# Optimization experiments

Hardware: AMD Instinct MI355X
Metric: run time of the kernel (lower is better)

The kernel has to match this reference:

```python
import jax, jax.numpy as jnp
import numpy as np
import math

DIM = 384; HEADS = 12; HD = 32; L_REL = 4; L_STD = 12; MLP_H = 4 * DIM
B = 8; N = 256
N_REL = 1
TIME_SCALE = 30000.0 / 500 * 0.3
SCALE = HD ** -0.5
NEG = -1e9  # finite stand-in for -inf padding mask (identical softmax result, safe grads)


def _ln(x, g, b):
    m = x.mean(-1, keepdims=True)
    v = ((x - m) ** 2).mean(-1, keepdims=True)
    return (x - m) / jnp.sqrt(v + 1e-5) * g + b


def _sin_emb(x, dim):
    half = dim // 2
    freq = jnp.exp(jnp.arange(half, dtype=x.dtype) * (-math.log(10000.0) / half))
    e = x[..., None] * freq
    return jnp.concatenate([jnp.sin(e), jnp.cos(e)], -1)


def _rel_bias(x0, w1d, b1d, wp, bp):
    pos = x0[..., :3]
    t = x0[..., 3:4]
    dpos = pos[:, :, None] - pos[:, None, :]                 # [B,N,N,3]
    dt = t[:, :, None] - t[:, None, :] * TIME_SCALE          # [B,N,N,1] (scale on 2nd term, as in torch)
    dpos2 = dpos ** 2
    dt2 = dt ** 2
    ds2 = dpos2.sum(-1) - dt2[..., 0]
    d = jnp.sign(ds2) * jnp.sqrt(jnp.abs(ds2))
    f = jnp.concatenate([dpos, dt, dpos2, dt2], -1)          # [B,N,N,8]
    d = d + (f @ w1d.T + b1d)[..., 0]
    emb = _sin_emb(1024.0 * jnp.clip(d, -4.0, 4.0), HD)      # [B,N,N,HD]
    return emb @ wp.T + bp


def _mask_bias(mask):
    mn = jnp.minimum(mask[:, None, :], mask[:, :, None])
    mx = jnp.maximum(mask[:, None, :], mask[:, :, None])
    return jnp.where(mx < 0, 0.0, mn)                        # [B,N,N]


def _attn(xq, xkv, wq, wk, wv, wo, bo, rel, mbias):
    Bq, Nq, _ = xq.shape
    q = (xq @ wq.T).reshape(Bq, Nq, HEADS, HD).transpose(0, 2, 1, 3) * SCALE
    k = (xkv @ wk.T).reshape(Bq, Nq, HEADS, HD).transpose(0, 2, 1, 3)
    v = (xkv @ wv.T).reshape(Bq, Nq, HEADS, HD).transpose(0, 2, 1, 3)
    a = jnp.einsum('bhic,bhjc->bhij', q, k)
    if rel is not None:
        a = a + jnp.einsum('bhic,bijc->bhij', q, rel)
    if mbias is not None:
        a = a + mbias[:, None]
    a = jax.nn.softmax(a, axis=-1)
    o = jnp.einsum('bhij,bhjc->bihc', a, v)
    if rel is not None:
        o = o + jnp.einsum('bhij,bijc->bihc', a, rel)
    return o.reshape(Bq, Nq, HEADS * HD) @ wo.T + bo


def _mlp(x, w1, b1, w2, b2):
    return jax.nn.gelu(x @ w1.T + b1, approximate=False) @ w2.T + b2


def setup_inputs() -> dict:
    key = jax.random.key(0)
    ks = iter(jax.random.split(key, 64))
    f = lambda shape: jax.random.normal(next(ks), shape, jnp.float32) * 0.02
    inp = {}
    inp['x'] = jax.random.normal(next(ks), (B, N, DIM), jnp.float32)
    inp['x0'] = jax.random.normal(next(ks), (B, N, 4), jnp.float32)
    lengths = jax.random.randint(next(ks), (B,), N // 2, N + 1)
    inp['mask'] = jnp.where(jnp.arange(N)[None, :] < lengths[:, None], 0.0, NEG).astype(jnp.float32)
    inp['rp_w1d'] = f((1, 8)); inp['rp_b1d'] = jnp.zeros((1,), jnp.float32)
    inp['rp_wp'] = f((HD, HD)); inp['rp_bp'] = jnp.zeros((HD,), jnp.float32)
    for p, L in (('sw', L_REL), ('bl', L_STD)):
        inp[p + '_ln1_g'] = jnp.ones((L, DIM), jnp.float32); inp[p + '_ln1_b'] = jnp.zeros((L, DIM), jnp.float32)
        inp[p + '_ln2_g'] = jnp.ones((L, DIM), jnp.float32); inp[p + '_ln2_b'] = jnp.zeros((L, DIM), jnp.float32)
        inp[p + '_wq'] = f((L, DIM, DIM)); inp[p + '_wk'] = f((L, DIM, DIM)); inp[p + '_wv'] = f((L, DIM, DIM))
        inp[p + '_wo'] = f((L, DIM, DIM)); inp[p + '_bo'] = jnp.zeros((L, DIM), jnp.float32)
        inp[p + '_w1'] = f((L, MLP_H, DIM)); inp[p + '_b1'] = jnp.zeros((L, MLP_H), jnp.float32)
        inp[p + '_w2'] = f((L, DIM, MLP_H)); inp[p + '_b2'] = jnp.zeros((L, DIM), jnp.float32)
    inp['bl_g1'] = jnp.ones((L_STD, DIM), jnp.float32)   # init_values=1
    inp['bl_g2'] = jnp.ones((L_STD, DIM), jnp.float32)
    inp['cls_w'] = f((DIM,))
    inp['out_w'] = f((3, DIM)); inp['out_b'] = jnp.zeros((3,), jnp.float32)
    return inp


def reference(x, x0, mask, rp_w1d, rp_b1d, rp_wp, rp_bp,
              sw_ln1_g, sw_ln1_b, sw_ln2_g, sw_ln2_b, sw_wq, sw_wk, sw_wv, sw_wo, sw_bo,
              sw_w1, sw_b1, sw_w2, sw_b2,
              bl_ln1_g, bl_ln1_b, bl_ln2_g, bl_ln2_b, bl_wq, bl_wk, bl_wv, bl_wo, bl_bo,
              bl_w1, bl_b1, bl_w2, bl_b2, bl_g1, bl_g2, cls_w, out_w, out_b):
    rel = _rel_bias(x0, rp_w1d, rp_b1d, rp_wp, rp_bp)
    mbias = _mask_bias(mask)
    for i in range(L_REL):
        r = rel if i < N_REL else None
        xn = _ln(x, sw_ln1_g[i], sw_ln1_b[i])
        x = x + _attn(xn, xn, sw_wq[i], sw_wk[i], sw_wv[i], sw_wo[i], sw_bo[i], r, mbias)
        x = x + _mlp(_ln(x, sw_ln2_g[i], sw_ln2_b[i]), sw_w1[i], sw_b1[i], sw_w2[i], sw_b2[i])
    # prepend cls token; it is always valid
    cls = jnp.broadcast_to(cls_w[None, None, :], (x.shape[0], 1, DIM))
    x = jnp.concatenate([cls, x], axis=1)
    mask2 = jnp.concatenate([jnp.zeros((x.shape[0], 1), mask.dtype), mask], axis=1)
    mbias2 = _mask_bias(mask2)
    for i in range(L_STD):
        xn = _ln(x, bl_ln1_g[i], bl_ln1_b[i])
        x = x + bl_g1[i] * _attn(xn, xn, bl_wq[i], bl_wk[i], bl_wv[i], bl_wo[i], bl_bo[i], None, mbias2)
        x = x + bl_g2[i] * _mlp(_ln(x, bl_ln2_g[i], bl_ln2_b[i]), bl_w1[i], bl_b1[i], bl_w2[i], bl_b2[i])
    return x[:, 0] @ out_w.T + out_b   # [B, 3]
```

## Files before the change

kernel.cpp:

```cpp
#include <hip/hip_runtime.h>
#include <hip/hip_bf16.h>
#include <math.h>

#define DIM 384
#define HEADS 12
#define HD 32
#define MLP_H 1536
#define BATCH 8
#define N1 256
#define N2 257
#define QP 1152
#define SCALE 0.17677669529663687f
#define TIME_SCALE 18.0f

typedef __attribute__((ext_vector_type(8))) short frag8;
typedef __attribute__((ext_vector_type(4))) float f32x4;

__device__ inline short f2bf(float x) {
    __hip_bfloat16 h = __float2bfloat16(x);
    short s;
    __builtin_memcpy(&s, &h, 2);
    return s;
}
__device__ inline float bf2f(short s) {
    unsigned u = ((unsigned)(unsigned short)s) << 16;
    float f;
    __builtin_memcpy(&f, &u, 4);
    return f;
}

__global__ __launch_bounds__(256) void conv_kernel(
        const float* __restrict__ in, short* __restrict__ out, int n) {
    int i = (blockIdx.x * 256 + threadIdx.x) * 4;
    if (i >= n) return;
    float4 v = *(const float4*)(in + i);
    out[i]     = f2bf(v.x);
    out[i + 1] = f2bf(v.y);
    out[i + 2] = f2bf(v.z);
    out[i + 3] = f2bf(v.w);
}

__global__ __launch_bounds__(256) void conv_qkv_kernel(
        const float* __restrict__ wq, const float* __restrict__ wk,
        const float* __restrict__ wv, short* __restrict__ out, int L) {
    size_t idx = ((size_t)blockIdx.x * 256 + threadIdx.x) * 4;
    size_t total = (size_t)L * QP * DIM;
    if (idx >= total) return;
    size_t k = idx % DIM;
    size_t row = idx / DIM;
    size_t r = row % QP;
    size_t l = row / QP;
    int which = (int)(r / DIM);
    int rr = (int)(r % DIM);
    const float* src = ((which == 0) ? wq : (which == 1) ? wk : wv)
                     + (l * DIM + rr) * DIM + k;
    float4 v = *(const float4*)src;
    out[idx]     = f2bf(v.x);
    out[idx + 1] = f2bf(v.y);
    out[idx + 2] = f2bf(v.z);
    out[idx + 3] = f2bf(v.w);
}

__global__ __launch_bounds__(256) void rel_kernel(
        const float* __restrict__ x0, const float* __restrict__ w1d,
        const float* __restrict__ b1d, const float* __restrict__ wp,
        const float* __restrict__ bp, short* __restrict__ rel) {
    __shared__ float swp[HD * HD];
    __shared__ float sbp[HD];
    __shared__ float sw1[8];
    __shared__ float sb1;
    __shared__ float sfreq[16];
    int tid = threadIdx.x;
    for (int i = tid; i < HD * HD; i += 256) swp[i] = wp[i];
    if (tid < HD) sbp[tid] = bp[tid];
    if (tid < 8) sw1[tid] = w1d[tid];
    if (tid == 0) sb1 = b1d[0];
    if (tid < 16) sfreq[tid] = expf(-(float)tid * 0.5756462732485114f);
    __syncthreads();

    int gid = blockIdx.x * 256 + tid;
    int j  = gid & (N1 - 1);
    int bi = gid >> 8;
    int i  = bi & (N1 - 1);
    int b  = bi >> 8;

    const float* pi = x0 + (size_t)(b * N1 + i) * 4;
    const float* pj = x0 + (size_t)(b * N1 + j) * 4;
    float dx = pi[0] - pj[0], dy = pi[1] - pj[1], dz = pi[2] - pj[2];
    float dt = pi[3] - pj[3] * TIME_SCALE;
    float dx2 = dx * dx, dy2 = dy * dy, dz2 = dz * dz, dt2 = dt * dt;
    float ds2 = dx2 + dy2 + dz2 - dt2;
    float d = copysignf(sqrtf(fabsf(ds2)), ds2);
    d += dx * sw1[0] + dy * sw1[1] + dz * sw1[2] + dt * sw1[3]
       + dx2 * sw1[4] + dy2 * sw1[5] + dz2 * sw1[6] + dt2 * sw1[7] + sb1;
    d = fminf(fmaxf(d, -4.f), 4.f) * 1024.f;

    float emb[32];
    #pragma unroll
    for (int k = 0; k < 16; k++) {
        float s, c;
        sincosf(d * sfreq[k], &s, &c);
        emb[k] = s; emb[16 + k] = c;
    }
    short* out = rel + (size_t)gid * HD;
    #pragma unroll 4
    for (int c = 0; c < HD; c++) {
        float a = sbp[c];
        #pragma unroll
        for (int k = 0; k < 32; k++) a += emb[k] * swp[c * 32 + k];
        out[c] = f2bf(a);
    }
}

__global__ __launch_bounds__(128) void ln_kernel(
        const float* __restrict__ x, const float* __restrict__ g,
        const float* __restrict__ b, short* __restrict__ y) {
    int r = blockIdx.x;
    int t = threadIdx.x;
    const float* xr = x + (size_t)r * DIM;
    float v0 = xr[t], v1 = xr[t + 128], v2 = xr[t + 256];
    __shared__ float redm[2], redv[2];
    float s = v0 + v1 + v2;
    for (int o = 32; o; o >>= 1) s += __shfl_down(s, o, 64);
    int lane = t & 63, wid = t >> 6;
    if (!lane) redm[wid] = s;
    __syncthreads();
    float mean = (redm[0] + redm[1]) * (1.f / DIM);
    float d0 = v0 - mean, d1 = v1 - mean, d2 = v2 - mean;
    float s2 = d0 * d0 + d1 * d1 + d2 * d2;
    for (int o = 32; o; o >>= 1) s2 += __shfl_down(s2, o, 64);
    if (!lane) redv[wid] = s2;
    __syncthreads();
    float var = (redv[0] + redv[1]) * (1.f / DIM);
    float rs = rsqrtf(var + 1e-5f);
    short* yr = y + (size_t)r * DIM;
    yr[t]       = f2bf(d0 * rs * g[t]       + b[t]);
    yr[t + 128] = f2bf(d1 * rs * g[t + 128] + b[t + 128]);
    yr[t + 256] = f2bf(d2 * rs * g[t + 256] + b[t + 256]);
}

__global__ __launch_bounds__(512) void gemm_bf16_kernel(
        const short* __restrict__ A, const short* __restrict__ W,
        const float* __restrict__ bias, const float* __restrict__ resid,
        const float* __restrict__ gvec, float* __restrict__ Cf,
        short* __restrict__ Cb, int M, int Np, int K, int mode) {
    __shared__ short As2[2][2][4][64][8];
    __shared__ short Bs2[2][2][4][64][8];
    int tid = threadIdx.x;
    int w = tid >> 6, lane = tid & 63;
    int nlo = lane & 15, quad = lane >> 4;
    int g = w >> 2, wl = w & 3;
    int wm = wl >> 1, wn = wl & 1;
    int n0 = blockIdx.x * 64, m0 = blockIdx.y * 64;

    f32x4 acc00 = {0.f, 0.f, 0.f, 0.f}, acc01 = {0.f, 0.f, 0.f, 0.f};
    f32x4 acc10 = {0.f, 0.f, 0.f, 0.f}, acc11 = {0.f, 0.f, 0.f, 0.f};

    int oct16 = tid & 15, rbase = tid >> 4;
    int kh_s = oct16 >> 3, oo = oct16 & 7, ks_s = oo >> 2, q_s = oo & 3;
    const frag8 fz = {0, 0, 0, 0, 0, 0, 0, 0};
    frag8 pa0 = fz, pa1 = fz, pb0, pb1;

    {
        int gm0 = m0 + rbase, gm1 = m0 + rbase + 32;
        if (gm0 < M) pa0 = *(const frag8*)(A + (size_t)gm0 * K + oct16 * 8);
        if (gm1 < M) pa1 = *(const frag8*)(A + (size_t)gm1 * K + oct16 * 8);
        pb0 = *(const frag8*)(W + (size_t)(n0 + rbase) * K + oct16 * 8);
        pb1 = *(const frag8*)(W + (size_t)(n0 + rbase + 32) * K + oct16 * 8);
    }

    for (int k0 = 0; k0 < K; k0 += 128) {
        *(frag8*)&As2[kh_s][ks_s][q_s][rbase][0]      = pa0;
        *(frag8*)&As2[kh_s][ks_s][q_s][rbase + 32][0] = pa1;
        *(frag8*)&Bs2[kh_s][ks_s][q_s][rbase][0]      = pb0;
        *(frag8*)&Bs2[kh_s][ks_s][q_s][rbase + 32][0] = pb1;
        __syncthreads();
        int kn = k0 + 128;
        if (kn < K) {
            int gm0 = m0 + rbase, gm1 = m0 + rbase + 32;
            pa0 = fz; pa1 = fz;
            if (gm0 < M) pa0 = *(const frag8*)(A + (size_t)gm0 * K + kn + oct16 * 8);
            if (gm1 < M) pa1 = *(const frag8*)(A + (size_t)gm1 * K + kn + oct16 * 8);
            pb0 = *(const frag8*)(W + (size_t)(n0 + rbase) * K + kn + oct16 * 8);
            pb1 = *(const frag8*)(W + (size_t)(n0 + rbase + 32) * K + kn + oct16 * 8);
        }
        #pragma unroll
        for (int ks = 0; ks < 2; ks++) {
            frag8 a0 = *(const frag8*)&As2[g][ks][quad][wm * 32 + nlo][0];
            frag8 a1 = *(const frag8*)&As2[g][ks][quad][wm * 32 + 16 + nlo][0];
            frag8 b0 = *(const frag8*)&Bs2[g][ks][quad][wn * 32 + nlo][0];
            frag8 b1 = *(const frag8*)&Bs2[g][ks][quad][wn * 32 + 16 + nlo][0];
            acc00 = __builtin_amdgcn_mfma_f32_16x16x32_bf16(a0, b0, acc00, 0, 0, 0);
            acc01 = __builtin_amdgcn_mfma_f32_16x16x32_bf16(a0, b1, acc01, 0, 0, 0);
            acc10 = __builtin_amdgcn_mfma_f32_16x16x32_bf16(a1, b0, acc10, 0, 0, 0);
            acc11 = __builtin_amdgcn_mfma_f32_16x16x32_bf16(a1, b1, acc11, 0, 0, 0);
        }
        __syncthreads();
    }

    f32x4* red4 = (f32x4*)&As2[0][0][0][0][0];
    int roff = wl * 64 + lane;
    if (g == 1) {
        red4[roff]       = acc00;
        red4[256 + roff] = acc01;
        red4[512 + roff] = acc10;
        red4[768 + roff] = acc11;
    }
    __syncthreads();
    if (g == 1) return;
    {
        f32x4 t0 = red4[roff], t1 = red4[256 + roff];
        f32x4 t2 = red4[512 + roff], t3 = red4[768 + roff];
        #pragma unroll
        for (int r = 0; r < 4; r++) {
            acc00[r] += t0[r]; acc01[r] += t1[r];
            acc10[r] += t2[r]; acc11[r] += t3[r];
        }
    }

    #pragma unroll
    for (int mi = 0; mi < 2; mi++) {
        #pragma unroll
        for (int nf = 0; nf < 2; nf++) {
            f32x4 av = (mi == 0) ? ((nf == 0) ? acc00 : acc01)
                                 : ((nf == 0) ? acc10 : acc11);
            int col = n0 + wn * 32 + nf * 16 + nlo;
            float bcol = (mode >= 1) ? bias[col] : 0.f;
            float gs = 1.f;
            if (mode == 2 && gvec) gs = gvec[col];
            #pragma unroll
            for (int r = 0; r < 4; r++) {
                int row = m0 + wm * 32 + mi * 16 + quad * 4 + r;
                if (row >= M) continue;
                float v = av[r] + bcol;
                if (mode == 1) v = 0.5f * v * (1.f + erff(v * 0.70710678118654752f));
                if (mode == 2) {
                    Cf[(size_t)row * Np + col] = resid[(size_t)row * Np + col] + gs * v;
                } else {
                    Cb[(size_t)row * Np + col] = f2bf(v);
                }
            }
        }
    }
}

__global__ __launch_bounds__(256) void attn_mfma_kernel(
        const short* __restrict__ qkv, const float* __restrict__ maskv,
        short* __restrict__ ob, int Nseq) {
    __shared__ short kf[18][64][8];
    __shared__ short vf[9][2][64][8];
    __shared__ short pbuf[4][16][40];
    __shared__ float ms[320];

    int tid = threadIdx.x;
    int w = tid >> 6, lane = tid & 63;
    int n = lane & 15, quad = lane >> 4;
    int qg = blockIdx.x, h = blockIdx.y, b = blockIdx.z;
    size_t rowB = (size_t)(b * Nseq);

    for (int j = tid; j < 320; j += 256)
        ms[j] = (j < Nseq) ? maskv[b * Nseq + j] : 0.f;

    {
        int c0 = (tid & 3) * 8;
        for (int j = tid >> 2; j < 288; j += 64) {
            frag8 kk = {0, 0, 0, 0, 0, 0, 0, 0};
            frag8 vv = {0, 0, 0, 0, 0, 0, 0, 0};
            if (j < Nseq) {
                const short* base = qkv + (rowB + j) * QP + h * HD + c0;
                kk = *(const frag8*)(base + 384);
                vv = *(const frag8*)(base + 768);
            }
            *(frag8*)&kf[j >> 4][(c0 >> 3) * 16 + (j & 15)][0] = kk;
            #pragma unroll
            for (int e = 0; e < 8; e++) {
                int c = c0 + e;
                vf[j >> 5][c >> 4][((j & 31) >> 3) * 16 + (c & 15)][j & 7] = vv[e];
            }
        }
    }

    int i0 = qg * 64 + w * 16;
    frag8 qa = {0, 0, 0, 0, 0, 0, 0, 0};
    {
        int i = i0 + n;
        if (i < Nseq) qa = *(const frag8*)(qkv + (rowB + i) * QP + h * HD + quad * 8);
    }
    __syncthreads();

    float msq[4];
    #pragma unroll
    for (int r = 0; r < 4; r++) msq[r] = ms[i0 + quad * 4 + r];

    float mrow[4], lsum[4];
    #pragma unroll
    for (int r = 0; r < 4; r++) { mrow[r] = -3.0e38f; lsum[r] = 0.f; }
    f32x4 oacc0 = {0.f, 0.f, 0.f, 0.f}, oacc1 = {0.f, 0.f, 0.f, 0.f};

    for (int jb = 0; jb < 9; jb++) {
        frag8 kb0 = *(const frag8*)&kf[2 * jb][lane][0];
        frag8 kb1 = *(const frag8*)&kf[2 * jb + 1][lane][0];
        f32x4 z = {0.f, 0.f, 0.f, 0.f};
        f32x4 s0 = __builtin_amdgcn_mfma_f32_16x16x32_bf16(qa, kb0, z, 0, 0, 0);
        f32x4 s1 = __builtin_amdgcn_mfma_f32_16x16x32_bf16(qa, kb1, z, 0, 0, 0);

        int j0 = jb * 32 + n;
        int j1 = j0 + 16;
        float mj0 = ms[j0], mj1 = ms[j1];
        float pad0 = (j0 < Nseq) ? 0.f : -1e9f;
        float pad1 = (j1 < Nseq) ? 0.f : -1e9f;

        #pragma unroll
        for (int r = 0; r < 4; r++) {
            float mi = msq[r];
            float b0 = ((fmaxf(mi, mj0) < 0.f) ? 0.f : fminf(mi, mj0)) + pad0;
            float b1 = ((fmaxf(mi, mj1) < 0.f) ? 0.f : fminf(mi, mj1)) + pad1;
            float v0 = s0[r] * SCALE + b0;
            float v1 = s1[r] * SCALE + b1;
            float rm = fmaxf(v0, v1);
            rm = fmaxf(rm, __shfl_xor(rm, 1));
            rm = fmaxf(rm, __shfl_xor(rm, 2));
            rm = fmaxf(rm, __shfl_xor(rm, 4));
            rm = fmaxf(rm, __shfl_xor(rm, 8));
            float mn = fmaxf(mrow[r], rm);
            float alpha = __expf(mrow[r] - mn);
            mrow[r] = mn;
            float p0 = __expf(v0 - mn);
            float p1 = __expf(v1 - mn);
            float ps = p0 + p1;
            ps += __shfl_xor(ps, 1);
            ps += __shfl_xor(ps, 2);
            ps += __shfl_xor(ps, 4);
            ps += __shfl_xor(ps, 8);
            lsum[r] = lsum[r] * alpha + ps;
            oacc0[r] *= alpha;
            oacc1[r] *= alpha;
            pbuf[w][quad * 4 + r][n]      = f2bf(p0);
            pbuf[w][quad * 4 + r][n + 16] = f2bf(p1);
        }
        __syncthreads();
        frag8 pa = *(const frag8*)&pbuf[w][n][quad * 8];
        frag8 vb0 = *(const frag8*)&vf[jb][0][lane][0];
        frag8 vb1 = *(const frag8*)&vf[jb][1][lane][0];
        oacc0 = __builtin_amdgcn_mfma_f32_16x16x32_bf16(pa, vb0, oacc0, 0, 0, 0);
        oacc1 = __builtin_amdgcn_mfma_f32_16x16x32_bf16(pa, vb1, oacc1, 0, 0, 0);
        __syncthreads();
    }

    #pragma unroll
    for (int r = 0; r < 4; r++) {
        int i = i0 + quad * 4 + r;
        if (i < Nseq) {
            float invl = 1.f / lsum[r];
            ob[(rowB + i) * DIM + h * HD + n]      = f2bf(oacc0[r] * invl);
            ob[(rowB + i) * DIM + h * HD + 16 + n] = f2bf(oacc1[r] * invl);
        }
    }
}

__global__ __launch_bounds__(256) void attn_rel_mfma_kernel(
        const short* __restrict__ qkv, const short* __restrict__ relb,
        const float* __restrict__ maskv, short* __restrict__ ob) {
    const int Nseq = N1;
    __shared__ short kf[16][64][8];
    __shared__ short vf[8][2][64][8];
    __shared__ short pbuf[4][16][40];
    __shared__ float qrow[4][16][32];
    __shared__ float orel[4][16][33];
    __shared__ float alphas[4][16];
    __shared__ float ms[256];

    int tid = threadIdx.x;
    int w = tid >> 6, lane = tid & 63;
    int n = lane & 15, quad = lane >> 4;
    int qg = blockIdx.x, h = blockIdx.y, b = blockIdx.z;
    size_t rowB = (size_t)(b * Nseq);

    if (tid < 256) ms[tid] = maskv[b * Nseq + tid];

    {
        int c0 = (tid & 3) * 8;
        for (int j = tid >> 2; j < 256; j += 64) {
            const short* base = qkv + (rowB + j) * QP + h * HD + c0;
            frag8 kk = *(const frag8*)(base + 384);
            frag8 vv = *(const frag8*)(base + 768);
            *(frag8*)&kf[j >> 4][(c0 >> 3) * 16 + (j & 15)][0] = kk;
            #pragma unroll
            for (int e = 0; e < 8; e++) {
                int c = c0 + e;
                vf[j >> 5][c >> 4][((j & 31) >> 3) * 16 + (c & 15)][j & 7] = vv[e];
            }
        }
    }

    int i0 = qg * 64 + w * 16;
    frag8 qa = *(const frag8*)(qkv + (rowB + i0 + n) * QP + h * HD + quad * 8);
    {
        int il = lane >> 2, c8 = (lane & 3) * 8;
        frag8 qv = *(const frag8*)(qkv + (rowB + i0 + il) * QP + h * HD + c8);
        #pragma unroll
        for (int e = 0; e < 8; e++) qrow[w][il][c8 + e] = bf2f(qv[e]) * SCALE;
    }
    __syncthreads();

    float msq[4];
    #pragma unroll
    for (int r = 0; r < 4; r++) msq[r] = ms[i0 + quad * 4 + r];

    float mrow[4], lsum[4];
    #pragma unroll
    for (int r = 0; r < 4; r++) { mrow[r] = -3.0e38f; lsum[r] = 0.f; }
    f32x4 oacc0 = {0.f, 0.f, 0.f, 0.f}, oacc1 = {0.f, 0.f, 0.f, 0.f};
    float arel[8];
    #pragma unroll
    for (int e = 0; e < 8; e++) arel[e] = 0.f;

    int il = lane & 15, oct = lane >> 4;
    const short* relrow = relb + (((size_t)b * N1 + (i0 + il)) * N1) * HD + oct * 8;

    for (int jb = 0; jb < 8; jb++) {
        frag8 kb0 = *(const frag8*)&kf[2 * jb][lane][0];
        frag8 kb1 = *(const frag8*)&kf[2 * jb + 1][lane][0];
        f32x4 z = {0.f, 0.f, 0.f, 0.f};
        f32x4 s0 = __builtin_amdgcn_mfma_f32_16x16x32_bf16(qa, kb0, z, 0, 0, 0);
        f32x4 s1 = __builtin_amdgcn_mfma_f32_16x16x32_bf16(qa, kb1, z, 0, 0, 0);

        int j0 = jb * 32 + n;
        int j1 = j0 + 16;
        float mj0 = ms[j0], mj1 = ms[j1];

        #pragma unroll
        for (int r = 0; r < 4; r++) {
            int i = i0 + quad * 4 + r;
            const short* r0 = relb + (((size_t)b * N1 + i) * N1 + j0) * HD;
            const short* r1 = relb + (((size_t)b * N1 + i) * N1 + j1) * HD;
            float d0 = 0.f, d1 = 0.f;
            #pragma unroll
            for (int c8 = 0; c8 < 4; c8++) {
                frag8 ra = *(const frag8*)(r0 + c8 * 8);
                frag8 rb_ = *(const frag8*)(r1 + c8 * 8);
                const float* qp = &qrow[w][quad * 4 + r][c8 * 8];
                #pragma unroll
                for (int e = 0; e < 8; e++) {
                    float qv = qp[e];
                    d0 += qv * bf2f(ra[e]);
                    d1 += qv * bf2f(rb_[e]);
                }
            }
            float mi = msq[r];
            float b0 = (fmaxf(mi, mj0) < 0.f) ? 0.f : fminf(mi, mj0);
            float b1 = (fmaxf(mi, mj1) < 0.f) ? 0.f : fminf(mi, mj1);
            float v0 = s0[r] * SCALE + d0 + b0;
            float v1 = s1[r] * SCALE + d1 + b1;
            float rm = fmaxf(v0, v1);
            rm = fmaxf(rm, __shfl_xor(rm, 1));
            rm = fmaxf(rm, __shfl_xor(rm, 2));
            rm = fmaxf(rm, __shfl_xor(rm, 4));
            rm = fmaxf(rm, __shfl_xor(rm, 8));
            float mn = fmaxf(mrow[r], rm);
            float alpha = __expf(mrow[r] - mn);
            mrow[r] = mn;
            float p0 = __expf(v0 - mn);
            float p1 = __expf(v1 - mn);
            float ps = p0 + p1;
            ps += __shfl_xor(ps, 1);
            ps += __shfl_xor(ps, 2);
            ps += __shfl_xor(ps, 4);
            ps += __shfl_xor(ps, 8);
            lsum[r] = lsum[r] * alpha + ps;
            oacc0[r] *= alpha;
            oacc1[r] *= alpha;
            pbuf[w][quad * 4 + r][n]      = f2bf(p0);
            pbuf[w][quad * 4 + r][n + 16] = f2bf(p1);
            if (n == 0) alphas[w][quad * 4 + r] = alpha;
        }
        __syncthreads();
        {
            float al = alphas[w][il];
            #pragma unroll
            for (int e = 0; e < 8; e++) arel[e] *= al;
            const short* rb2 = relrow + (size_t)(jb * 32) * HD;
            #pragma unroll 8
            for (int jj = 0; jj < 32; jj++) {
                float p = bf2f(pbuf[w][il][jj]);
                frag8 rv = *(const frag8*)(rb2 + (size_t)jj * HD);
                #pragma unroll
                for (int e = 0; e < 8; e++) arel[e] += p * bf2f(rv[e]);
            }
        }
        frag8 pa = *(const frag8*)&pbuf[w][n][quad * 8];
        frag8 vb0 = *(const frag8*)&vf[jb][0][lane][0];
        frag8 vb1 = *(const frag8*)&vf[jb][1][lane][0];
        oacc0 = __builtin_amdgcn_mfma_f32_16x16x32_bf16(pa, vb0, oacc0, 0, 0, 0);
        oacc1 = __builtin_amdgcn_mfma_f32_16x16x32_bf16(pa, vb1, oacc1, 0, 0, 0);
        __syncthreads();
    }

    #pragma unroll
    for (int e = 0; e < 8; e++) orel[w][il][oct * 8 + e] = arel[e];
    __syncthreads();

    #pragma unroll
    for (int r = 0; r < 4; r++) {
        int i = i0 + quad * 4 + r;
        float invl = 1.f / lsum[r];
        float o0 = (oacc0[r] + orel[w][quad * 4 + r][n])      * invl;
        float o1 = (oacc1[r] + orel[w][quad * 4 + r][16 + n]) * invl;
        ob[(rowB + i) * DIM + h * HD + n]      = f2bf(o0);
        ob[(rowB + i) * DIM + h * HD + 16 + n] = f2bf(o1);
    }
}

__global__ __launch_bounds__(256) void concat_kernel(
        const float* __restrict__ xa, const float* __restrict__ clsw,
        const float* __restrict__ mask, float* __restrict__ xb,
        float* __restrict__ m2) {
    int idx = blockIdx.x * 256 + threadIdx.x;
    const int total = BATCH * N2 * DIM;
    if (idx < total) {
        int c = idx % DIM;
        int tokb = idx / DIM;
        int p = tokb % N2, b = tokb / N2;
        xb[idx] = (p == 0) ? clsw[c] : xa[((size_t)(b * N1) + p - 1) * DIM + c];
    }
    if (idx < BATCH * N2) {
        int p = idx % N2, b = idx / N2;
        m2[idx] = (p == 0) ? 0.f : mask[b * N1 + p - 1];
    }
}

__global__ __launch_bounds__(64) void head_kernel(
        const float* __restrict__ xb, const float* __restrict__ ow,
        const float* __restrict__ obv, float* __restrict__ out) {
    int blk = blockIdx.x;
    int b = blk / 3, o = blk % 3;
    int lane = threadIdx.x;
    const float* xr = xb + (size_t)(b * N2) * DIM;
    const float* wr = ow + o * DIM;
    float s = 0.f;
    for (int c = lane; c < DIM; c += 64) s += xr[c] * wr[c];
    for (int off = 32; off; off >>= 1) s += __shfl_down(s, off, 64);
    if (!lane) out[blk] = s + obv[o];
}

extern "C" void kernel_launch(void* const* d_in, const int* in_sizes, int n_in,
                              void* d_out, int out_size, void* d_ws, size_t ws_size,
                              hipStream_t stream) {
    (void)in_sizes; (void)n_in; (void)out_size; (void)ws_size;
    const float* X       = (const float*)d_in[0];
    const float* X0      = (const float*)d_in[1];
    const float* MSK     = (const float*)d_in[2];
    const float* RW1     = (const float*)d_in[3];
    const float* RB1     = (const float*)d_in[4];
    const float* RWP     = (const float*)d_in[5];
    const float* RBP     = (const float*)d_in[6];
    const float* SW_LN1G = (const float*)d_in[7];
    const float* SW_LN1B = (const float*)d_in[8];
    const float* SW_LN2G = (const float*)d_in[9];
    const float* SW_LN2B = (const float*)d_in[10];
    const float* SW_WQ   = (const float*)d_in[11];
    const float* SW_WK   = (const float*)d_in[12];
    const float* SW_WV   = (const float*)d_in[13];
    const float* SW_WO   = (const float*)d_in[14];
    const float* SW_BO   = (const float*)d_in[15];
    const float* SW_W1   = (const float*)d_in[16];
    const float* SW_B1   = (const float*)d_in[17];
    const float* SW_W2   = (const float*)d_in[18];
    const float* SW_B2   = (const float*)d_in[19];
    const float* BL_LN1G = (const float*)d_in[20];
    const float* BL_LN1B = (const float*)d_in[21];
    const float* BL_LN2G = (const float*)d_in[22];
    const float* BL_LN2B = (const float*)d_in[23];
    const float* BL_WQ   = (const float*)d_in[24];
    const float* BL_WK   = (const float*)d_in[25];
    const float* BL_WV   = (const float*)d_in[26];
    const float* BL_WO   = (const float*)d_in[27];
    const float* BL_BO   = (const float*)d_in[28];
    const float* BL_W1   = (const float*)d_in[29];
    const float* BL_B1   = (const float*)d_in[30];
    const float* BL_W2   = (const float*)d_in[31];
    const float* BL_B2   = (const float*)d_in[32];
    const float* BL_G1   = (const float*)d_in[33];
    const float* BL_G2   = (const float*)d_in[34];
    const float* CLSW    = (const float*)d_in[35];
    const float* OUTW    = (const float*)d_in[36];
    const float* OUTB    = (const float*)d_in[37];

    const int T1 = BATCH * N1;
    const int T2 = BATCH * N2;
    const size_t RELSZ = (size_t)BATCH * N1 * N1 * HD;

    short* rel = (short*)d_ws;
    float* xa  = (float*)(rel + RELSZ);
    float* xb  = xa + (size_t)T1 * DIM;
    float* m2  = xb + (size_t)T2 * DIM;
    short* sbase = (short*)(m2 + 2064);
    short* xn   = sbase;
    short* qkv  = xn  + (size_t)T2 * DIM;
    short* ab   = qkv + (size_t)T2 * QP;
    short* hb   = ab  + (size_t)T2 * DIM;
    short* cw_qkv_sw = hb + (size_t)T2 * MLP_H;
    short* cw_qkv_bl = cw_qkv_sw + (size_t)4  * QP * DIM;
    short* cw_wo_sw  = cw_qkv_bl + (size_t)12 * QP * DIM;
    short* cw_wo_bl  = cw_wo_sw  + (size_t)4  * DIM * DIM;
    short* cw_w1_sw  = cw_wo_bl  + (size_t)12 * DIM * DIM;
    short* cw_w1_bl  = cw_w1_sw  + (size_t)4  * MLP_H * DIM;
    short* cw_w2_sw  = cw_w1_bl  + (size_t)12 * MLP_H * DIM;
    short* cw_w2_bl  = cw_w2_sw  + (size_t)4  * DIM * MLP_H;

    conv_qkv_kernel<<<(4 * QP * DIM / 4 + 255) / 256, 256, 0, stream>>>(SW_WQ, SW_WK, SW_WV, cw_qkv_sw, 4);
    conv_qkv_kernel<<<(12 * QP * DIM / 4 + 255) / 256, 256, 0, stream>>>(BL_WQ, BL_WK, BL_WV, cw_qkv_bl, 12);
    conv_kernel<<<(4 * DIM * DIM / 4 + 255) / 256, 256, 0, stream>>>(SW_WO, cw_wo_sw, 4 * DIM * DIM);
    conv_kernel<<<(12 * DIM * DIM / 4 + 255) / 256, 256, 0, stream>>>(BL_WO, cw_wo_bl, 12 * DIM * DIM);
    conv_kernel<<<(4 * MLP_H * DIM / 4 + 255) / 256, 256, 0, stream>>>(SW_W1, cw_w1_sw, 4 * MLP_H * DIM);
    conv_kernel<<<(12 * MLP_H * DIM / 4 + 255) / 256, 256, 0, stream>>>(BL_W1, cw_w1_bl, 12 * MLP_H * DIM);
    conv_kernel<<<(4 * DIM * MLP_H / 4 + 255) / 256, 256, 0, stream>>>(SW_W2, cw_w2_sw, 4 * DIM * MLP_H);
    conv_kernel<<<(12 * DIM * MLP_H / 4 + 255) / 256, 256, 0, stream>>>(BL_W2, cw_w2_bl, 12 * DIM * MLP_H);

    rel_kernel<<<BATCH * N1 * N1 / 256, 256, 0, stream>>>(X0, RW1, RB1, RWP, RBP, rel);
    hipMemcpyAsync(xa, X, sizeof(float) * T1 * DIM, hipMemcpyDeviceToDevice, stream);

    dim3 gQ1(QP / 64, T1 / 64);
    dim3 gP1(DIM / 64, T1 / 64);
    dim3 gM1(MLP_H / 64, T1 / 64);
    dim3 gF1(4, HEADS, BATCH);
    for (int l = 0; l < 4; l++) {
        const short* wqkv = cw_qkv_sw + (size_t)l * QP * DIM;
        const short* wo = cw_wo_sw + (size_t)l * DIM * DIM;
        const short* w1 = cw_w1_sw + (size_t)l * MLP_H * DIM;
        const short* w2 = cw_w2_sw + (size_t)l * DIM * MLP_H;
        const float* bo = SW_BO + (size_t)l * DIM;
        const float* b1 = SW_B1 + (size_t)l * MLP_H;
        const float* b2 = SW_B2 + (size_t)l * DIM;

        ln_kernel<<<T1, 128, 0, stream>>>(xa, SW_LN1G + l * DIM, SW_LN1B + l * DIM, xn);
        gemm_bf16_kernel<<<gQ1, 512, 0, stream>>>(xn, wqkv, nullptr, nullptr, nullptr,
                                                  nullptr, qkv, T1, QP, DIM, 0);
        if (l == 0)
            attn_rel_mfma_kernel<<<gF1, 256, 0, stream>>>(qkv, rel, MSK, ab);
        else
            attn_mfma_kernel<<<gF1, 256, 0, stream>>>(qkv, MSK, ab, N1);
        gemm_bf16_kernel<<<gP1, 512, 0, stream>>>(ab, wo, bo, xa, nullptr,
                                                  xa, nullptr, T1, DIM, DIM, 2);
        ln_kernel<<<T1, 128, 0, stream>>>(xa, SW_LN2G + l * DIM, SW_LN2B + l * DIM, xn);
        gemm_bf16_kernel<<<gM1, 512, 0, stream>>>(xn, w1, b1, nullptr, nullptr,
                                                  nullptr, hb, T1, MLP_H, DIM, 1);
        gemm_bf16_kernel<<<gP1, 512, 0, stream>>>(hb, w2, b2, xa, nullptr,
                                                  xa, nullptr, T1, DIM, MLP_H, 2);
    }

    concat_kernel<<<(BATCH * N2 * DIM + 255) / 256, 256, 0, stream>>>(xa, CLSW, MSK, xb, m2);

    int MB2 = (T2 + 63) / 64;
    dim3 gQ2(QP / 64, MB2);
    dim3 gP2(DIM / 64, MB2);
    dim3 gM2(MLP_H / 64, MB2);
    dim3 gF2(5, HEADS, BATCH);
    for (int l = 0; l < 12; l++) {
        const short* wqkv = cw_qkv_bl + (size_t)l * QP * DIM;
        const short* wo = cw_wo_bl + (size_t)l * DIM * DIM;
        const short* w1 = cw_w1_bl + (size_t)l * MLP_H * DIM;
        const short* w2 = cw_w2_bl + (size_t)l * DIM * MLP_H;
        const float* bo = BL_BO + (size_t)l * DIM;
        const float* b1 = BL_B1 + (size_t)l * MLP_H;
        const float* b2 = BL_B2 + (size_t)l * DIM;
        const float* g1 = BL_G1 + (size_t)l * DIM;
        const float* g2 = BL_G2 + (size_t)l * DIM;

        ln_kernel<<<T2, 128, 0, stream>>>(xb, BL_LN1G + l * DIM, BL_LN1B + l * DIM, xn);
        gemm_bf16_kernel<<<gQ2, 512, 0, stream>>>(xn, wqkv, nullptr, nullptr, nullptr,
                                                  nullptr, qkv, T2, QP, DIM, 0);
        attn_mfma_kernel<<<gF2, 256, 0, stream>>>(qkv, m2, ab, N2);
        gemm_bf16_kernel<<<gP2, 512, 0, stream>>>(ab, wo, bo, xb, g1,
                                                  xb, nullptr, T2, DIM, DIM, 2);
        ln_kernel<<<T2, 128, 0, stream>>>(xb, BL_LN2G + l * DIM, BL_LN2B + l * DIM, xn);
        gemm_bf16_kernel<<<gM2, 512, 0, stream>>>(xn, w1, b1, nullptr, nullptr,
                                                  nullptr, hb, T2, MLP_H, DIM, 1);
        gemm_bf16_kernel<<<gP2, 512, 0, stream>>>(hb, w2, b2, xb, g2,
                                                  xb, nullptr, T2, DIM, MLP_H, 2);
    }

    head_kernel<<<BATCH * 3, 64, 0, stream>>>(xb, OUTW, OUTB, (float*)d_out);
}
```

Before: 1.832 ms.

## Fuse LayerNorm into QKV and MLP-up GEMMs; use wave barriers in attention

```diff
diff --git a/kernel.cpp b/kernel.cpp
--- a/kernel.cpp
+++ b/kernel.cpp
@@ -112,31 +112,142 @@
     }
 }
 
-__global__ __launch_bounds__(128) void ln_kernel(
-        const float* __restrict__ x, const float* __restrict__ g,
-        const float* __restrict__ b, short* __restrict__ y) {
-    int r = blockIdx.x;
-    int t = threadIdx.x;
-    const float* xr = x + (size_t)r * DIM;
-    float v0 = xr[t], v1 = xr[t + 128], v2 = xr[t + 256];
-    __shared__ float redm[2], redv[2];
-    float s = v0 + v1 + v2;
-    for (int o = 32; o; o >>= 1) s += __shfl_down(s, o, 64);
-    int lane = t & 63, wid = t >> 6;
-    if (!lane) redm[wid] = s;
+__global__ __launch_bounds__(512) void gemm_ln_bf16_kernel(
+        const float* __restrict__ Af, const float* __restrict__ gamma,
+        const float* __restrict__ beta, const short* __restrict__ W,
+        const float* __restrict__ bias, short* __restrict__ Cb,
+        int M, int Np, int do_gelu) {
+    __shared__ short As3[3][2][2][4][64][8];
+    __shared__ short Bs[2][2][4][64][8];
+    __shared__ float gs[384], bs[384];
+    __shared__ float psum[64][9], psq[64][9];
+    int tid = threadIdx.x;
+    int w = tid >> 6, lane = tid & 63;
+    int nlo = lane & 15, quad = lane >> 4;
+    int gq = w >> 2, wl = w & 3;
+    int wm = wl >> 1, wn = wl & 1;
+    int n0 = blockIdx.x * 64, m0 = blockIdx.y * 64;
+
+    if (tid < 384) { gs[tid] = gamma[tid]; bs[tid] = beta[tid]; }
+
+    int row = tid >> 3, seg = tid & 7;
+    int gm = m0 + row;
+    {
+        float s = 0.f, s2 = 0.f;
+        if (gm < M) {
+            const float* src = Af + (size_t)gm * 384 + seg * 48;
+            #pragma unroll
+            for (int t = 0; t < 12; t++) {
+                float4 v4 = *(const float4*)(src + t * 4);
+                s += v4.x + v4.y + v4.z + v4.w;
+                s2 += v4.x * v4.x + v4.y * v4.y + v4.z * v4.z + v4.w * v4.w;
+            }
+        }
+        psum[row][seg] = s; psq[row][seg] = s2;
+    }
     __syncthreads();
-    float mean = (redm[0] + redm[1]) * (1.f / DIM);
-    float d0 = v0 - mean, d1 = v1 - mean, d2 = v2 - mean;
-    float s2 = d0 * d0 + d1 * d1 + d2 * d2;
-    for (int o = 32; o; o >>= 1) s2 += __shfl_down(s2, o, 64);
-    if (!lane) redv[wid] = s2;
+    float mean, rs;
+    {
+        float s = 0.f, s2 = 0.f;
+        #pragma unroll
+        for (int t = 0; t < 8; t++) { s += psum[row][t]; s2 += psq[row][t]; }
+        mean = s * (1.f / 384.f);
+        float var = s2 * (1.f / 384.f) - mean * mean;
+        rs = rsqrtf(var + 1e-5f);
+    }
+    {
+        const frag8 fz = {0, 0, 0, 0, 0, 0, 0, 0};
+        const float* src = Af + (size_t)gm * 384 + seg * 48;
+        #pragma unroll
+        for (int o = 0; o < 6; o++) {
+            int kb = seg * 48 + o * 8;
+            frag8 fv = fz;
+            if (gm < M) {
+                float4 va = *(const float4*)(src + o * 8);
+                float4 vb = *(const float4*)(src + o * 8 + 4);
+                fv[0] = f2bf((va.x - mean) * rs * gs[kb + 0] + bs[kb + 0]);
+                fv[1] = f2bf((va.y - mean) * rs * gs[kb + 1] + bs[kb + 1]);
+                fv[2] = f2bf((va.z - mean) * rs * gs[kb + 2] + bs[kb + 2]);
+                fv[3] = f2bf((va.w - mean) * rs * gs[kb + 3] + bs[kb + 3]);
+                fv[4] = f2bf((vb.x - mean) * rs * gs[kb + 4] + bs[kb + 4]);
+                fv[5] = f2bf((vb.y - mean) * rs * gs[kb + 5] + bs[kb + 5]);
+                fv[6] = f2bf((vb.z - mean) * rs * gs[kb + 6] + bs[kb + 6]);
+                fv[7] = f2bf((vb.w - mean) * rs * gs[kb + 7] + bs[kb + 7]);
+            }
+            int oct = (kb & 127) >> 3;
+            *(frag8*)&As3[kb >> 7][oct >> 3][(oct & 7) >> 2][oct & 3][row][0] = fv;
+        }
+    }
+
+    int oct16 = tid & 15, rb = tid >> 4;
+    int kh_s = oct16 >> 3, oo = oct16 & 7, ks_s = oo >> 2, q_s = oo & 3;
+    frag8 pb0 = *(const frag8*)(W + (size_t)(n0 + rb) * 384 + oct16 * 8);
+    frag8 pb1 = *(const frag8*)(W + (size_t)(n0 + rb + 32) * 384 + oct16 * 8);
+
+    f32x4 acc00 = {0.f, 0.f, 0.f, 0.f}, acc01 = {0.f, 0.f, 0.f, 0.f};
+    f32x4 acc10 = {0.f, 0.f, 0.f, 0.f}, acc11 = {0.f, 0.f, 0.f, 0.f};
+
     __syncthreads();
-    float var = (redv[0] + redv[1]) * (1.f / DIM);
-    float rs = rsqrtf(var + 1e-5f);
-    short* yr = y + (size_t)r * DIM;
-    yr[t]       = f2bf(d0 * rs * g[t]       + b[t]);
-    yr[t + 128] = f2bf(d1 * rs * g[t + 128] + b[t + 128]);
-    yr[t + 256] = f2bf(d2 * rs * g[t + 256] + b[t + 256]);
+    for (int c = 0; c < 3; c++) {
+        *(frag8*)&Bs[kh_s][ks_s][q_s][rb][0]      = pb0;
+        *(frag8*)&Bs[kh_s][ks_s][q_s][rb + 32][0] = pb1;
+        __syncthreads();
+        if (c < 2) {
+            pb0 = *(const frag8*)(W + (size_t)(n0 + rb) * 384 + (c + 1) * 128 + oct16 * 8);
+            pb1 = *(const frag8*)(W + (size_t)(n0 + rb + 32) * 384 + (c + 1) * 128 + oct16 * 8);
+        }
+        #pragma unroll
+        for (int ks = 0; ks < 2; ks++) {
+            frag8 a0 = *(const frag8*)&As3[c][gq][ks][quad][wm * 32 + nlo][0];
+            frag8 a1 = *(const frag8*)&As3[c][gq][ks][quad][wm * 32 + 16 + nlo][0];
+            frag8 b0 = *(const frag8*)&Bs[gq][ks][quad][wn * 32 + nlo][0];
+            frag8 b1 = *(const frag8*)&Bs[gq][ks][quad][wn * 32 + 16 + nlo][0];
+            acc00 = __builtin_amdgcn_mfma_f32_16x16x32_bf16(a0, b0, acc00, 0, 0, 0);
+            acc01 = __builtin_amdgcn_mfma_f32_16x16x32_bf16(a0, b1, acc01, 0, 0, 0);
+            acc10 = __builtin_amdgcn_mfma_f32_16x16x32_bf16(a1, b0, acc10, 0, 0, 0);
+            acc11 = __builtin_amdgcn_mfma_f32_16x16x32_bf16(a1, b1, acc11, 0, 0, 0);
+        }
+        __syncthreads();
+    }
+
+    f32x4* red4 = (f32x4*)&Bs[0][0][0][0][0];
+    int roff = wl * 64 + lane;
+    if (gq == 1) {
+        red4[roff]       = acc00;
+        red4[256 + roff] = acc01;
+        red4[512 + roff] = acc10;
+        red4[768 + roff] = acc11;
+    }
+    __syncthreads();
+    if (gq == 1) return;
+    {
+        f32x4 t0 = red4[roff], t1 = red4[256 + roff];
+        f32x4 t2 = red4[512 + roff], t3 = red4[768 + roff];
+        #pragma unroll
+        for (int r = 0; r < 4; r++) {
+            acc00[r] += t0[r]; acc01[r] += t1[r];
+            acc10[r] += t2[r]; acc11[r] += t3[r];
+        }
+    }
+
+    #pragma unroll
+    for (int mi = 0; mi < 2; mi++) {
+        #pragma unroll
+        for (int nf = 0; nf < 2; nf++) {
+            f32x4 av = (mi == 0) ? ((nf == 0) ? acc00 : acc01)
+                                 : ((nf == 0) ? acc10 : acc11);
+            int col = n0 + wn * 32 + nf * 16 + nlo;
+            float bcol = bias ? bias[col] : 0.f;
+            #pragma unroll
+            for (int r = 0; r < 4; r++) {
+                int orow = m0 + wm * 32 + mi * 16 + quad * 4 + r;
+                if (orow >= M) continue;
+                float v = av[r] + bcol;
+                if (do_gelu) v = 0.5f * v * (1.f + erff(v * 0.70710678118654752f));
+                Cb[(size_t)orow * Np + col] = f2bf(v);
+            }
+        }
+    }
 }
 
 __global__ __launch_bounds__(512) void gemm_bf16_kernel(
@@ -338,13 +449,13 @@
             pbuf[w][quad * 4 + r][n]      = f2bf(p0);
             pbuf[w][quad * 4 + r][n + 16] = f2bf(p1);
         }
-        __syncthreads();
+        __builtin_amdgcn_wave_barrier();
         frag8 pa = *(const frag8*)&pbuf[w][n][quad * 8];
         frag8 vb0 = *(const frag8*)&vf[jb][0][lane][0];
         frag8 vb1 = *(const frag8*)&vf[jb][1][lane][0];
         oacc0 = __builtin_amdgcn_mfma_f32_16x16x32_bf16(pa, vb0, oacc0, 0, 0, 0);
         oacc1 = __builtin_amdgcn_mfma_f32_16x16x32_bf16(pa, vb1, oacc1, 0, 0, 0);
-        __syncthreads();
+        __builtin_amdgcn_wave_barrier();
     }
 
     #pragma unroll
@@ -474,7 +585,7 @@
             pbuf[w][quad * 4 + r][n + 16] = f2bf(p1);
             if (n == 0) alphas[w][quad * 4 + r] = alpha;
         }
-        __syncthreads();
+        __builtin_amdgcn_wave_barrier();
         {
             float al = alphas[w][il];
             #pragma unroll
@@ -493,12 +604,12 @@
         frag8 vb1 = *(const frag8*)&vf[jb][1][lane][0];
         oacc0 = __builtin_amdgcn_mfma_f32_16x16x32_bf16(pa, vb0, oacc0, 0, 0, 0);
         oacc1 = __builtin_amdgcn_mfma_f32_16x16x32_bf16(pa, vb1, oacc1, 0, 0, 0);
-        __syncthreads();
+        __builtin_amdgcn_wave_barrier();
     }
 
     #pragma unroll
     for (int e = 0; e < 8; e++) orel[w][il][oct * 8 + e] = arel[e];
-    __syncthreads();
+    __builtin_amdgcn_wave_barrier();
 
     #pragma unroll
     for (int r = 0; r < 4; r++) {
@@ -595,8 +706,7 @@
     float* xb  = xa + (size_t)T1 * DIM;
     float* m2  = xb + (size_t)T2 * DIM;
     short* sbase = (short*)(m2 + 2064);
-    short* xn   = sbase;
-    short* qkv  = xn  + (size_t)T2 * DIM;
+    short* qkv  = sbase;
     short* ab   = qkv + (size_t)T2 * QP;
     short* hb   = ab  + (size_t)T2 * DIM;
     short* cw_qkv_sw = hb + (size_t)T2 * MLP_H;
@@ -633,18 +743,16 @@
         const float* b1 = SW_B1 + (size_t)l * MLP_H;
         const float* b2 = SW_B2 + (size_t)l * DIM;
 
-        ln_kernel<<<T1, 128, 0, stream>>>(xa, SW_LN1G + l * DIM, SW_LN1B + l * DIM, xn);
-        gemm_bf16_kernel<<<gQ1, 512, 0, stream>>>(xn, wqkv, nullptr, nullptr, nullptr,
-                                                  nullptr, qkv, T1, QP, DIM, 0);
+        gemm_ln_bf16_kernel<<<gQ1, 512, 0, stream>>>(
+            xa, SW_LN1G + l * DIM, SW_LN1B + l * DIM, wqkv, nullptr, qkv, T1, QP, 0);
         if (l == 0)
             attn_rel_mfma_kernel<<<gF1, 256, 0, stream>>>(qkv, rel, MSK, ab);
         else
             attn_mfma_kernel<<<gF1, 256, 0, stream>>>(qkv, MSK, ab, N1);
         gemm_bf16_kernel<<<gP1, 512, 0, stream>>>(ab, wo, bo, xa, nullptr,
                                                   xa, nullptr, T1, DIM, DIM, 2);
-        ln_kernel<<<T1, 128, 0, stream>>>(xa, SW_LN2G + l * DIM, SW_LN2B + l * DIM, xn);
-        gemm_bf16_kernel<<<gM1, 512, 0, stream>>>(xn, w1, b1, nullptr, nullptr,
-                                                  nullptr, hb, T1, MLP_H, DIM, 1);
+        gemm_ln_bf16_kernel<<<gM1, 512, 0, stream>>>(
+            xa, SW_LN2G + l * DIM, SW_LN2B + l * DIM, w1, b1, hb, T1, MLP_H, 1);
         gemm_bf16_kernel<<<gP1, 512, 0, stream>>>(hb, w2, b2, xa, nullptr,
                                                   xa, nullptr, T1, DIM, MLP_H, 2);
     }
@@ -667,15 +775,13 @@
         const float* g1 = BL_G1 + (size_t)l * DIM;
         const float* g2 = BL_G2 + (size_t)l * DIM;
 
-        ln_kernel<<<T2, 128, 0, stream>>>(xb, BL_LN1G + l * DIM, BL_LN1B + l * DIM, xn);
-        gemm_bf16_kernel<<<gQ2, 512, 0, stream>>>(xn, wqkv, nullptr, nullptr, nullptr,
-                                                  nullptr, qkv, T2, QP, DIM, 0);
+        gemm_ln_bf16_kernel<<<gQ2, 512, 0, stream>>>(
+            xb, BL_LN1G + l * DIM, BL_LN1B + l * DIM, wqkv, nullptr, qkv, T2, QP, 0);
         attn_mfma_kernel<<<gF2, 256, 0, stream>>>(qkv, m2, ab, N2);
         gemm_bf16_kernel<<<gP2, 512, 0, stream>>>(ab, wo, bo, xb, g1,
                                                   xb, nullptr, T2, DIM, DIM, 2);
-        ln_kernel<<<T2, 128, 0, stream>>>(xb, BL_LN2G + l * DIM, BL_LN2B + l * DIM, xn);
-        gemm_bf16_kernel<<<gM2, 512, 0, stream>>>(xn, w1, b1, nullptr, nullptr,
-                                                  nullptr, hb, T2, MLP_H, DIM, 1);
+        gemm_ln_bf16_kernel<<<gM2, 512, 0, stream>>>(
+            xb, BL_LN2G + l * DIM, BL_LN2B + l * DIM, w1, b1, hb, T2, MLP_H, 1);
         gemm_bf16_kernel<<<gP2, 512, 0, stream>>>(hb, w2, b2, xb, g2,
                                                   xb, nullptr, T2, DIM, MLP_H, 2);
     }
```

Result: slower. 2.066 ms (+12.8%).
